# Performance work log

Measured on AMD Instinct MI355X. Metric: run time of the kernel, lower is better.

## Reference

```python
import math
import jax, jax.numpy as jnp
import numpy as np

D_K = 64

def setup_inputs() -> dict:
    key = jax.random.key(0)
    kq, kk, kv = jax.random.split(key, 3)
    shape = (2, 16, 2048, D_K)  # [batch, heads, seq, d_k]
    return {
        "query": jax.random.normal(kq, shape, dtype=jnp.float32),
        "key": jax.random.normal(kk, shape, dtype=jnp.float32),
        "value": jax.random.normal(kv, shape, dtype=jnp.float32),
    }

def reference(query, key, value):
    # scores: [b, h, s_q, s_k]
    scores = jnp.einsum("bhqd,bhkd->bhqk", query, key) / math.sqrt(D_K)
    # max-subtract (explicit in original; jax.nn.softmax is already stable,
    # but subtracting first matches the original math exactly)
    scores = scores - jnp.max(scores, axis=-1, keepdims=True)
    weights = jax.nn.softmax(scores, axis=-1)
    # dropout is identity in eval/reference mode
    output = jnp.einsum("bhqk,bhkd->bhqd", weights, value)
    return (output, weights)
```

## Files before the change

kernel.cpp:

```cpp
#include <hip/hip_runtime.h>

#define S 2048
#define D 64
#define BH 32
#define BR 64
#define BC 64
#define NTILES (S / BC)

typedef __attribute__((ext_vector_type(8))) short bf16x8;
typedef __attribute__((ext_vector_type(4))) float f32x4;

__device__ __forceinline__ unsigned short f2bf(float f) {
    union { float f; unsigned u; } v; v.f = f;
    unsigned u = v.u;
    return (unsigned short)((u + 0x7FFFu + ((u >> 16) & 1u)) >> 16);
}

__device__ __forceinline__ void stage8k(const unsigned short* g, unsigned short* l, int t) {
    const char* gp = (const char*)g + t * 16;
    char* lp = (char*)l + t * 16;
    __builtin_amdgcn_global_load_lds((const __attribute__((address_space(1))) void*)gp,
                                     (__attribute__((address_space(3))) void*)lp, 16, 0, 0);
    __builtin_amdgcn_global_load_lds((const __attribute__((address_space(1))) void*)(gp + 4096),
                                     (__attribute__((address_space(3))) void*)(lp + 4096), 16, 0, 0);
}

__global__ __launch_bounds__(256) void prep_tiles(const float* __restrict__ kin,
                                                  const float* __restrict__ vin,
                                                  unsigned short* __restrict__ kb,
                                                  unsigned short* __restrict__ vtb) {
    __shared__ float lt[64 * 67];
    const int bh = blockIdx.y, tile = blockIdx.x, t = threadIdx.x;
    if (blockIdx.z == 0) {
        const float* src = kin + ((size_t)bh * S + tile * 64) * D;
        unsigned short* dst = kb + ((size_t)(bh * NTILES + tile) << 12);
#pragma unroll
        for (int i = 0; i < 2; ++i) {
            const int ob = (i * 256 + t) * 16;
            const int row = ob >> 7;
            const int c0 = ((ob & 127) ^ ((row & 7) << 4)) >> 1;
            const float4 f0 = *(const float4*)(src + row * D + c0);
            const float4 f1 = *(const float4*)(src + row * D + c0 + 4);
            bf16x8 h;
            h[0]=(short)f2bf(f0.x); h[1]=(short)f2bf(f0.y); h[2]=(short)f2bf(f0.z); h[3]=(short)f2bf(f0.w);
            h[4]=(short)f2bf(f1.x); h[5]=(short)f2bf(f1.y); h[6]=(short)f2bf(f1.z); h[7]=(short)f2bf(f1.w);
            *(bf16x8*)((char*)dst + ob) = h;
        }
    } else {
        const float* src = vin + ((size_t)bh * S + tile * 64) * D;
#pragma unroll
        for (int i = 0; i < 4; ++i) {
            const int idx = i * 256 + t;
            const int r = idx >> 4, c4 = (idx & 15) * 4;
            const float4 f = *(const float4*)(src + r * D + c4);
            lt[r * 67 + c4 + 0] = f.x; lt[r * 67 + c4 + 1] = f.y;
            lt[r * 67 + c4 + 2] = f.z; lt[r * 67 + c4 + 3] = f.w;
        }
        __syncthreads();
        unsigned short* dst = vtb + ((size_t)(bh * NTILES + tile) << 12);
#pragma unroll
        for (int i = 0; i < 2; ++i) {
            const int ob = (i * 256 + t) * 16;
            const int drow = ob >> 7;
            const int k0 = ((ob & 127) ^ ((drow & 7) << 4)) >> 1;
            bf16x8 h;
#pragma unroll
            for (int j = 0; j < 8; ++j) h[j] = (short)f2bf(lt[(k0 + j) * 67 + drow]);
            *(bf16x8*)((char*)dst + ob) = h;
        }
    }
}

__global__ __launch_bounds__(256, 4) void attn_fused(const float* __restrict__ q,
        const unsigned short* __restrict__ kb, const unsigned short* __restrict__ vtb,
        float* __restrict__ o, float* __restrict__ w) {
    __shared__ unsigned short Kt[2][4096];
    __shared__ unsigned short Vt[2][4096];
    __shared__ unsigned short Pt[4096];

    const int id = blockIdx.x;
    const int bh = ((id & 7) << 2) + (id >> 8);
    const int qt = (id >> 3) & 31;
    const int q0 = qt * BR;
    const int t = threadIdx.x, lane = t & 63, wave = t >> 6;
    const int quad = lane >> 4, n = lane & 15;

    const int sw = (n & 7) << 4;
    const int cb0 = (quad * 16) ^ sw;
    const int cb1 = (64 + quad * 16) ^ sw;
    const int rb = n * 128;

    bf16x8 aq[2];
    {
        const float* qrow = q + ((size_t)bh * S + q0 + wave * 16 + n) * D + quad * 8;
#pragma unroll
        for (int c = 0; c < 2; ++c) {
            const float4 f0 = *(const float4*)(qrow + c * 32);
            const float4 f1 = *(const float4*)(qrow + c * 32 + 4);
            bf16x8 a;
            a[0]=(short)f2bf(f0.x*0.125f); a[1]=(short)f2bf(f0.y*0.125f);
            a[2]=(short)f2bf(f0.z*0.125f); a[3]=(short)f2bf(f0.w*0.125f);
            a[4]=(short)f2bf(f1.x*0.125f); a[5]=(short)f2bf(f1.y*0.125f);
            a[6]=(short)f2bf(f1.z*0.125f); a[7]=(short)f2bf(f1.w*0.125f);
            aq[c] = a;
        }
    }

    const unsigned short* ktiles = kb + ((size_t)(bh * NTILES) << 12);
    const unsigned short* vtiles = vtb + ((size_t)(bh * NTILES) << 12);

    stage8k(ktiles, Kt[0], t);
    __syncthreads();
    float l_r[4] = {0.f, 0.f, 0.f, 0.f};
    for (int kc = 0; kc < NTILES; ++kc) {
        const int cur = kc & 1;
        if (kc + 1 < NTILES) stage8k(ktiles + ((size_t)(kc + 1) << 12), Kt[cur ^ 1], t);
        const char* kt = (const char*)Kt[cur];
#pragma unroll
        for (int nt = 0; nt < 4; ++nt) {
            f32x4 a = {0.f, 0.f, 0.f, 0.f};
            const bf16x8 b0 = *(const bf16x8*)(kt + nt * 2048 + rb + cb0);
            a = __builtin_amdgcn_mfma_f32_16x16x32_bf16(aq[0], b0, a, 0, 0, 0);
            const bf16x8 b1 = *(const bf16x8*)(kt + nt * 2048 + rb + cb1);
            a = __builtin_amdgcn_mfma_f32_16x16x32_bf16(aq[1], b1, a, 0, 0, 0);
#pragma unroll
            for (int r = 0; r < 4; ++r) l_r[r] += __expf(a[r]);
        }
        __syncthreads();
    }
#pragma unroll
    for (int msk = 1; msk <= 8; msk <<= 1)
#pragma unroll
        for (int r = 0; r < 4; ++r) l_r[r] += __shfl_xor(l_r[r], msk, 64);
    float rl[4];
#pragma unroll
    for (int r = 0; r < 4; ++r) rl[r] = 1.0f / l_r[r];

    stage8k(ktiles, Kt[0], t);
    stage8k(vtiles, Vt[0], t);
    __syncthreads();

    f32x4 accO[4] = {{0.f,0.f,0.f,0.f},{0.f,0.f,0.f,0.f},{0.f,0.f,0.f,0.f},{0.f,0.f,0.f,0.f}};
    float* wbase = w + ((size_t)bh * S + q0 + wave * 16 + quad * 4) * S + n;
    char* const pt = (char*)Pt;
    const int pw0 = wave * 2048;

    for (int kc = 0; kc < NTILES; ++kc) {
        const int cur = kc & 1;
        if (kc + 1 < NTILES) {
            stage8k(ktiles + ((size_t)(kc + 1) << 12), Kt[cur ^ 1], t);
            stage8k(vtiles + ((size_t)(kc + 1) << 12), Vt[cur ^ 1], t);
        }
        const char* kt = (const char*)Kt[cur];
        const char* vt = (const char*)Vt[cur];
        float* wp = wbase + kc * BC;
#pragma unroll
        for (int nt = 0; nt < 4; ++nt) {
            f32x4 a = {0.f, 0.f, 0.f, 0.f};
            const bf16x8 b0 = *(const bf16x8*)(kt + nt * 2048 + rb + cb0);
            a = __builtin_amdgcn_mfma_f32_16x16x32_bf16(aq[0], b0, a, 0, 0, 0);
            const bf16x8 b1 = *(const bf16x8*)(kt + nt * 2048 + rb + cb1);
            a = __builtin_amdgcn_mfma_f32_16x16x32_bf16(aq[1], b1, a, 0, 0, 0);
#pragma unroll
            for (int r = 0; r < 4; ++r) {
                const float pr = __expf(a[r]) * rl[r];
                __builtin_nontemporal_store(pr, wp + (size_t)r * S + nt * 16);
                const int prow = quad * 4 + r;
                *(unsigned short*)(pt + pw0 + prow * 128
                        + ((nt * 32 + 2 * n) ^ ((prow & 7) << 4))) = f2bf(pr);
            }
        }
#pragma unroll
        for (int c = 0; c < 2; ++c) {
            const bf16x8 ap = *(const bf16x8*)(pt + pw0 + rb + (c ? cb1 : cb0));
#pragma unroll
            for (int nt = 0; nt < 4; ++nt) {
                const bf16x8 bv = *(const bf16x8*)(vt + nt * 2048 + rb + (c ? cb1 : cb0));
                accO[nt] = __builtin_amdgcn_mfma_f32_16x16x32_bf16(ap, bv, accO[nt], 0, 0, 0);
            }
        }
        __syncthreads();
    }

    const size_t obase = ((size_t)bh * S + q0 + wave * 16 + quad * 4) * D + n;
#pragma unroll
    for (int nt = 0; nt < 4; ++nt)
#pragma unroll
        for (int r = 0; r < 4; ++r)
            __builtin_nontemporal_store(accO[nt][r], o + obase + (size_t)r * D + nt * 16);
}

extern "C" void kernel_launch(void* const* d_in, const int* in_sizes, int n_in,
                              void* d_out, int out_size, void* d_ws, size_t ws_size,
                              hipStream_t stream) {
    const float* q = (const float*)d_in[0];
    const float* k = (const float*)d_in[1];
    const float* v = (const float*)d_in[2];
    float* o = (float*)d_out;
    float* w = o + (size_t)BH * S * D;

    unsigned short* kb = (unsigned short*)d_ws;
    unsigned short* vtb = kb + (size_t)BH * S * D;

    dim3 pgrid(NTILES, BH, 2);
    prep_tiles<<<pgrid, dim3(256), 0, stream>>>(k, v, kb, vtb);
    attn_fused<<<dim3(1024), dim3(256), 0, stream>>>(q, kb, vtb, o, w);
}
```

Measured before the change: 672.1 us.

## Load K/V tiles directly into registers instead of staging through LDS

K and V bf16 tiles are now read from global memory straight into per-wave registers, with software double-buffering in the normalisation pass. The LDS double buffers, the async global-to-LDS staging and the per-tile block barriers are removed. The prep kernel stores the tiles in a plain, unswizzled layout to match the new fragment addressing. The aim is to remove barrier stalls and LDS traffic, at the cost of each wave loading the same K/V data separately from cache and using more registers.

```diff
diff --git a/kernel.cpp b/kernel.cpp
--- a/kernel.cpp
+++ b/kernel.cpp
@@ -16,15 +16,6 @@
     return (unsigned short)((u + 0x7FFFu + ((u >> 16) & 1u)) >> 16);
 }
 
-__device__ __forceinline__ void stage8k(const unsigned short* g, unsigned short* l, int t) {
-    const char* gp = (const char*)g + t * 16;
-    char* lp = (char*)l + t * 16;
-    __builtin_amdgcn_global_load_lds((const __attribute__((address_space(1))) void*)gp,
-                                     (__attribute__((address_space(3))) void*)lp, 16, 0, 0);
-    __builtin_amdgcn_global_load_lds((const __attribute__((address_space(1))) void*)(gp + 4096),
-                                     (__attribute__((address_space(3))) void*)(lp + 4096), 16, 0, 0);
-}
-
 __global__ __launch_bounds__(256) void prep_tiles(const float* __restrict__ kin,
                                                   const float* __restrict__ vin,
                                                   unsigned short* __restrict__ kb,
@@ -32,19 +23,17 @@
     __shared__ float lt[64 * 67];
     const int bh = blockIdx.y, tile = blockIdx.x, t = threadIdx.x;
     if (blockIdx.z == 0) {
-        const float* src = kin + ((size_t)bh * S + tile * 64) * D;
+        const float* src = kin + ((size_t)(bh * NTILES + tile) << 12);
         unsigned short* dst = kb + ((size_t)(bh * NTILES + tile) << 12);
 #pragma unroll
         for (int i = 0; i < 2; ++i) {
-            const int ob = (i * 256 + t) * 16;
-            const int row = ob >> 7;
-            const int c0 = ((ob & 127) ^ ((row & 7) << 4)) >> 1;
-            const float4 f0 = *(const float4*)(src + row * D + c0);
-            const float4 f1 = *(const float4*)(src + row * D + c0 + 4);
+            const int idx = i * 256 + t;
+            const float4 f0 = *(const float4*)(src + idx * 8);
+            const float4 f1 = *(const float4*)(src + idx * 8 + 4);
             bf16x8 h;
             h[0]=(short)f2bf(f0.x); h[1]=(short)f2bf(f0.y); h[2]=(short)f2bf(f0.z); h[3]=(short)f2bf(f0.w);
             h[4]=(short)f2bf(f1.x); h[5]=(short)f2bf(f1.y); h[6]=(short)f2bf(f1.z); h[7]=(short)f2bf(f1.w);
-            *(bf16x8*)((char*)dst + ob) = h;
+            *(bf16x8*)(dst + idx * 8) = h;
         }
     } else {
         const float* src = vin + ((size_t)bh * S + tile * 64) * D;
@@ -60,13 +49,13 @@
         unsigned short* dst = vtb + ((size_t)(bh * NTILES + tile) << 12);
 #pragma unroll
         for (int i = 0; i < 2; ++i) {
-            const int ob = (i * 256 + t) * 16;
-            const int drow = ob >> 7;
-            const int k0 = ((ob & 127) ^ ((drow & 7) << 4)) >> 1;
+            const int idx = i * 256 + t;
+            const int drow = idx >> 3;
+            const int k0 = (idx & 7) * 8;
             bf16x8 h;
 #pragma unroll
             for (int j = 0; j < 8; ++j) h[j] = (short)f2bf(lt[(k0 + j) * 67 + drow]);
-            *(bf16x8*)((char*)dst + ob) = h;
+            *(bf16x8*)(dst + idx * 8) = h;
         }
     }
 }
@@ -74,8 +63,6 @@
 __global__ __launch_bounds__(256, 4) void attn_fused(const float* __restrict__ q,
         const unsigned short* __restrict__ kb, const unsigned short* __restrict__ vtb,
         float* __restrict__ o, float* __restrict__ w) {
-    __shared__ unsigned short Kt[2][4096];
-    __shared__ unsigned short Vt[2][4096];
     __shared__ unsigned short Pt[4096];
 
     const int id = blockIdx.x;
@@ -85,10 +72,7 @@
     const int t = threadIdx.x, lane = t & 63, wave = t >> 6;
     const int quad = lane >> 4, n = lane & 15;
 
-    const int sw = (n & 7) << 4;
-    const int cb0 = (quad * 16) ^ sw;
-    const int cb1 = (64 + quad * 16) ^ sw;
-    const int rb = n * 128;
+    const int fo = n * 128 + quad * 16;
 
     bf16x8 aq[2];
     {
@@ -106,27 +90,41 @@
         }
     }
 
-    const unsigned short* ktiles = kb + ((size_t)(bh * NTILES) << 12);
-    const unsigned short* vtiles = vtb + ((size_t)(bh * NTILES) << 12);
+    const char* kt0 = (const char*)(kb + ((size_t)bh << 17));
+    const char* vt0 = (const char*)(vtb + ((size_t)bh << 17));
 
-    stage8k(ktiles, Kt[0], t);
-    __syncthreads();
+#define LK(base, f) do {                                              \
+    const char* _b = (base);                                          \
+    _Pragma("unroll")                                                 \
+    for (int _nt = 0; _nt < 4; ++_nt) {                               \
+        (f)[2*_nt]   = *(const bf16x8*)(_b + _nt*2048 + fo);          \
+        (f)[2*_nt+1] = *(const bf16x8*)(_b + _nt*2048 + fo + 64);     \
+    } } while (0)
+
     float l_r[4] = {0.f, 0.f, 0.f, 0.f};
-    for (int kc = 0; kc < NTILES; ++kc) {
-        const int cur = kc & 1;
-        if (kc + 1 < NTILES) stage8k(ktiles + ((size_t)(kc + 1) << 12), Kt[cur ^ 1], t);
-        const char* kt = (const char*)Kt[cur];
+    {
+        bf16x8 ka[8], kbf[8];
+        LK(kt0, ka);
+        for (int kc = 0; kc < NTILES; kc += 2) {
+            LK(kt0 + (kc + 1) * 8192, kbf);
 #pragma unroll
-        for (int nt = 0; nt < 4; ++nt) {
-            f32x4 a = {0.f, 0.f, 0.f, 0.f};
-            const bf16x8 b0 = *(const bf16x8*)(kt + nt * 2048 + rb + cb0);
-            a = __builtin_amdgcn_mfma_f32_16x16x32_bf16(aq[0], b0, a, 0, 0, 0);
-            const bf16x8 b1 = *(const bf16x8*)(kt + nt * 2048 + rb + cb1);
-            a = __builtin_amdgcn_mfma_f32_16x16x32_bf16(aq[1], b1, a, 0, 0, 0);
+            for (int nt = 0; nt < 4; ++nt) {
+                f32x4 a = {0.f, 0.f, 0.f, 0.f};
+                a = __builtin_amdgcn_mfma_f32_16x16x32_bf16(aq[0], ka[2*nt],   a, 0, 0, 0);
+                a = __builtin_amdgcn_mfma_f32_16x16x32_bf16(aq[1], ka[2*nt+1], a, 0, 0, 0);
 #pragma unroll
-            for (int r = 0; r < 4; ++r) l_r[r] += __expf(a[r]);
+                for (int r = 0; r < 4; ++r) l_r[r] += __expf(a[r]);
+            }
+            if (kc + 2 < NTILES) LK(kt0 + (kc + 2) * 8192, ka);
+#pragma unroll
+            for (int nt = 0; nt < 4; ++nt) {
+                f32x4 a = {0.f, 0.f, 0.f, 0.f};
+                a = __builtin_amdgcn_mfma_f32_16x16x32_bf16(aq[0], kbf[2*nt],   a, 0, 0, 0);
+                a = __builtin_amdgcn_mfma_f32_16x16x32_bf16(aq[1], kbf[2*nt+1], a, 0, 0, 0);
+#pragma unroll
+                for (int r = 0; r < 4; ++r) l_r[r] += __expf(a[r]);
+            }
         }
-        __syncthreads();
     }
 #pragma unroll
     for (int msk = 1; msk <= 8; msk <<= 1)
@@ -136,31 +134,24 @@
 #pragma unroll
     for (int r = 0; r < 4; ++r) rl[r] = 1.0f / l_r[r];
 
-    stage8k(ktiles, Kt[0], t);
-    stage8k(vtiles, Vt[0], t);
-    __syncthreads();
-
     f32x4 accO[4] = {{0.f,0.f,0.f,0.f},{0.f,0.f,0.f,0.f},{0.f,0.f,0.f,0.f},{0.f,0.f,0.f,0.f}};
     float* wbase = w + ((size_t)bh * S + q0 + wave * 16 + quad * 4) * S + n;
     char* const pt = (char*)Pt;
     const int pw0 = wave * 2048;
+    const int psw = (n & 7) << 4;
+    const int pA0 = (quad * 16) ^ psw;
+    const int pA1 = (64 + quad * 16) ^ psw;
 
     for (int kc = 0; kc < NTILES; ++kc) {
-        const int cur = kc & 1;
-        if (kc + 1 < NTILES) {
-            stage8k(ktiles + ((size_t)(kc + 1) << 12), Kt[cur ^ 1], t);
-            stage8k(vtiles + ((size_t)(kc + 1) << 12), Vt[cur ^ 1], t);
-        }
-        const char* kt = (const char*)Kt[cur];
-        const char* vt = (const char*)Vt[cur];
+        bf16x8 kf[8], vf[8];
+        LK(kt0 + kc * 8192, kf);
+        LK(vt0 + kc * 8192, vf);
         float* wp = wbase + kc * BC;
 #pragma unroll
         for (int nt = 0; nt < 4; ++nt) {
             f32x4 a = {0.f, 0.f, 0.f, 0.f};
-            const bf16x8 b0 = *(const bf16x8*)(kt + nt * 2048 + rb + cb0);
-            a = __builtin_amdgcn_mfma_f32_16x16x32_bf16(aq[0], b0, a, 0, 0, 0);
-            const bf16x8 b1 = *(const bf16x8*)(kt + nt * 2048 + rb + cb1);
-            a = __builtin_amdgcn_mfma_f32_16x16x32_bf16(aq[1], b1, a, 0, 0, 0);
+            a = __builtin_amdgcn_mfma_f32_16x16x32_bf16(aq[0], kf[2*nt],   a, 0, 0, 0);
+            a = __builtin_amdgcn_mfma_f32_16x16x32_bf16(aq[1], kf[2*nt+1], a, 0, 0, 0);
 #pragma unroll
             for (int r = 0; r < 4; ++r) {
                 const float pr = __expf(a[r]) * rl[r];
@@ -172,14 +163,11 @@
         }
 #pragma unroll
         for (int c = 0; c < 2; ++c) {
-            const bf16x8 ap = *(const bf16x8*)(pt + pw0 + rb + (c ? cb1 : cb0));
+            const bf16x8 ap = *(const bf16x8*)(pt + pw0 + n * 128 + (c ? pA1 : pA0));
 #pragma unroll
-            for (int nt = 0; nt < 4; ++nt) {
-                const bf16x8 bv = *(const bf16x8*)(vt + nt * 2048 + rb + (c ? cb1 : cb0));
-                accO[nt] = __builtin_amdgcn_mfma_f32_16x16x32_bf16(ap, bv, accO[nt], 0, 0, 0);
-            }
+            for (int nt = 0; nt < 4; ++nt)
+                accO[nt] = __builtin_amdgcn_mfma_f32_16x16x32_bf16(ap, vf[2*nt+c], accO[nt], 0, 0, 0);
         }
-        __syncthreads();
     }
 
     const size_t obase = ((size_t)bh * S + q0 + wave * 16 + quad * 4) * D + n;
```

Result: slower. 828.2 us (+23.2%).
